# Performance work log

Measured on AMD Instinct MI355X. Metric: run time of the kernel, lower is better.

## Reference

```python
import jax, jax.numpy as jnp
import numpy as np

N, E, G = 30000, 240000, 128
D_IN, D_H, D_OUT, HEADS = 128, 128, 16, 4
EPS_BN = 1e-5


def setup_inputs() -> dict:
    key = jax.random.key(0)
    ks = jax.random.split(key, 24)
    s = 0.1
    inp = {
        "x": jax.random.normal(ks[0], (N, D_IN), jnp.float32),
        "edge_index": jax.random.randint(ks[1], (2, E), 0, N, jnp.int32),
        "batch": jnp.sort(jax.random.randint(ks[2], (N,), 0, G, jnp.int32)),
        # stacked per-layer params (3 GAT blocks, identical shapes since D_IN==D_H)
        "W": jax.random.normal(ks[3], (3, D_H, HEADS * D_H), jnp.float32) * s,
        "att_src": jax.random.normal(ks[4], (3, HEADS, D_H), jnp.float32) * s,
        "att_dst": jax.random.normal(ks[5], (3, HEADS, D_H), jnp.float32) * s,
        "conv_b": jnp.zeros((3, D_H), jnp.float32),
        "gamma": jnp.ones((3, D_H), jnp.float32),
        "beta": jnp.zeros((3, D_H), jnp.float32),
        "sk_Win": jax.random.normal(ks[6], (3, D_H, D_H), jnp.float32) * s,
        "sk_bin": jnp.zeros((3, D_H), jnp.float32),
        "sk_Wout": jax.random.normal(ks[7], (3, D_H, D_H), jnp.float32) * s,
        "sk_bout": jnp.zeros((3, D_H), jnp.float32),
        "fc1_W": jax.random.normal(ks[8], (D_H, D_H), jnp.float32) * s,
        "fc1_b": jnp.zeros((D_H,), jnp.float32),
        "fc3_W": jax.random.normal(ks[9], (D_H, D_OUT), jnp.float32) * s,
        "fc3_b": jnp.zeros((D_OUT,), jnp.float32),
    }
    return inp


def _gat_conv(x, src, dst, W, a_src, a_dst, b):
    # PyG GATConv, heads=4, concat=False (mean over heads), leaky_relu 0.2
    h = (x @ W).reshape(N, HEADS, D_H)                      # [N,H,C]
    al_s = jnp.einsum('nhc,hc->nh', h, a_src)               # [N,H]
    al_d = jnp.einsum('nhc,hc->nh', h, a_dst)
    e = jax.nn.leaky_relu(al_s[src] + al_d[dst], 0.2)       # [Etot,H]
    m = jax.ops.segment_max(e, dst, num_segments=N)
    m = jnp.where(jnp.isfinite(m), m, 0.0)
    ex = jnp.exp(e - m[dst])
    z = jax.ops.segment_sum(ex, dst, num_segments=N)
    alpha = ex / (z[dst] + 1e-16)                           # [Etot,H]
    msg = h[src] * alpha[:, :, None]                        # [Etot,H,C]
    out = jax.ops.segment_sum(msg, dst, num_segments=N)     # [N,H,C]
    return out.mean(axis=1) + b


def _batch_norm(h, gamma, beta):
    mu = h.mean(axis=0)
    var = h.var(axis=0)
    return gamma * (h - mu) * jax.lax.rsqrt(var + EPS_BN) + beta


def _gated_skip(in_x, out_x, Win, bin_, Wout, bout):
    gate = jax.nn.sigmoid(in_x @ Win + bin_ + out_x @ Wout + bout)
    return gate * out_x + (1.0 - gate) * in_x


def reference(x, edge_index, batch, W, att_src, att_dst, conv_b, gamma, beta,
              sk_Win, sk_bin, sk_Wout, sk_bout, fc1_W, fc1_b, fc3_W, fc3_b):
    # add self loops (PyG GATConv default)
    loops = jnp.arange(N, dtype=edge_index.dtype)
    src = jnp.concatenate([edge_index[0], loops])
    dst = jnp.concatenate([edge_index[1], loops])

    h = x
    for l in range(3):
        idn = h
        h = _gat_conv(h, src, dst, W[l], att_src[l], att_dst[l], conv_b[l])
        h = _batch_norm(h, gamma[l], beta[l])
        h = _gated_skip(idn, h, sk_Win[l], sk_bin[l], sk_Wout[l], sk_bout[l])
        h = jax.nn.relu(h)

    # global mean pool over graphs
    cnt = jax.ops.segment_sum(jnp.ones((N,), h.dtype), batch, num_segments=G)
    hg = jax.ops.segment_sum(h, batch, num_segments=G) / jnp.maximum(cnt, 1.0)[:, None]
    hg = jax.nn.relu(hg @ fc1_W + fc1_b)
    return hg @ fc3_W + fc3_b
```

## Files before the change

### kernel.cpp

```cpp
#include <hip/hip_runtime.h>
#include <hip/hip_bf16.h>

#define N_NODES 30000
#define N_EDGES 240000
#define ETOT    (N_EDGES + N_NODES)
#define NGRAPH  128
#define NBLK    118

typedef __attribute__((ext_vector_type(8))) short bf16x8;
typedef __attribute__((ext_vector_type(4))) short bf16x4;
typedef __attribute__((ext_vector_type(4))) float f32x4;

__device__ __forceinline__ unsigned short f2bf(float f) {
    unsigned u = __float_as_uint(f);
    u += 0x7fff + ((u >> 16) & 1);
    return (unsigned short)(u >> 16);
}
__device__ __forceinline__ float bf2f(unsigned short h) {
    return __uint_as_float(((unsigned)h) << 16);
}

__global__ __launch_bounds__(256) void prep_kernel(const float* __restrict__ W,
                                                   const float* __restrict__ Win,
                                                   const float* __restrict__ Wout,
                                                   const float* __restrict__ x,
                                                   const int* __restrict__ batch,
                                                   short* __restrict__ wt_hi,
                                                   short* __restrict__ wint_hi,
                                                   short* __restrict__ woutt_hi,
                                                   short* __restrict__ xb,
                                                   int* __restrict__ gstart) {
    int i = blockIdx.x * 256 + threadIdx.x;
    if (i < 196608) {
        int l = i >> 16, r = i & 65535;
        int n = r >> 7, k = r & 127;
        wt_hi[i] = (short)f2bf(W[(size_t)l * 65536 + k * 512 + n]);
    } else if (i < 245760) {
        int j = i - 196608;
        int l = j >> 14, r = j & 16383;
        int n = r >> 7, k = r & 127;
        wint_hi[j] = (short)f2bf(Win[(size_t)l * 16384 + k * 128 + n]);
    } else if (i < 294912) {
        int j = i - 245760;
        int l = j >> 14, r = j & 16383;
        int n = r >> 7, k = r & 127;
        woutt_hi[j] = (short)f2bf(Wout[(size_t)l * 16384 + k * 128 + n]);
    } else if (i < 294912 + 480000) {
        int j = i - 294912;
        const float4* p = (const float4*)x + (size_t)j * 2;
        float4 v0 = p[0], v1 = p[1];
        bf16x8 hv;
        hv[0] = (short)f2bf(v0.x); hv[1] = (short)f2bf(v0.y);
        hv[2] = (short)f2bf(v0.z); hv[3] = (short)f2bf(v0.w);
        hv[4] = (short)f2bf(v1.x); hv[5] = (short)f2bf(v1.y);
        hv[6] = (short)f2bf(v1.z); hv[7] = (short)f2bf(v1.w);
        *(bf16x8*)(xb + (size_t)j * 8) = hv;
    } else if (i < 294912 + 480000 + 129) {
        int t = i - 294912 - 480000;
        int lo = 0, hi = N_NODES;
        while (lo < hi) { int mid = (lo + hi) >> 1; if (batch[mid] < t) lo = mid + 1; else hi = mid; }
        gstart[t] = lo;
    }
}

__global__ __launch_bounds__(256) void gemm_conv(const short* __restrict__ Ab,
                                                 const short* __restrict__ Bth,
                                                 const float* __restrict__ att_s,
                                                 const float* __restrict__ att_d,
                                                 unsigned short* __restrict__ hfullb,
                                                 float* __restrict__ als,
                                                 float* __restrict__ ald) {
    __shared__ short As_h[64 * 136];
    __shared__ float red_s[2][64], red_d[2][64];
    const int bm = blockIdx.x * 64;
    const int hd = blockIdx.y;
    const int bn = hd * 128;
    const int t  = threadIdx.x;
#pragma unroll
    for (int i = 0; i < 4; i++) {
        int idx8 = t + i * 256;
        int row = idx8 >> 4, c8 = (idx8 & 15) << 3;
        bf16x8 vh = {};
        if (bm + row < N_NODES)
            vh = *(const bf16x8*)(Ab + (size_t)(bm + row) * 128 + c8);
        *(bf16x8*)(As_h + row * 136 + c8) = vh;
    }
    __syncthreads();

    const int w = t >> 6, lane = t & 63;
    const int wr = w >> 1, wc = w & 1;
    const int lr = lane & 15, lg = lane >> 4;
    f32x4 acc[2][4] = {};
    const size_t bofs0 = (size_t)(bn + wc * 64 + lr) * 128 + lg * 8;
#pragma unroll
    for (int kk = 0; kk < 4; kk++) {
        bf16x8 ah[2], bh[4];
#pragma unroll
        for (int ni = 0; ni < 4; ni++) {
            size_t o = bofs0 + (size_t)ni * 16 * 128 + kk * 32;
            bh[ni] = *(const bf16x8*)(Bth + o);
        }
        int ko = kk * 32 + lg * 8;
#pragma unroll
        for (int mi = 0; mi < 2; mi++) {
            int r = wr * 32 + mi * 16 + lr;
            ah[mi] = *(const bf16x8*)(As_h + r * 136 + ko);
        }
#pragma unroll
        for (int mi = 0; mi < 2; mi++)
#pragma unroll
            for (int ni = 0; ni < 4; ni++)
                acc[mi][ni] = __builtin_amdgcn_mfma_f32_16x16x32_bf16(ah[mi], bh[ni], acc[mi][ni], 0, 0, 0);
    }
    float as_c[4], ad_c[4];
#pragma unroll
    for (int ni = 0; ni < 4; ni++) {
        int cc = wc * 64 + ni * 16 + lr;
        as_c[ni] = att_s[hd * 128 + cc];
        ad_c[ni] = att_d[hd * 128 + cc];
    }
#pragma unroll
    for (int mi = 0; mi < 2; mi++) {
#pragma unroll
        for (int r = 0; r < 4; r++) {
            float ps = 0.f, pd = 0.f;
#pragma unroll
            for (int ni = 0; ni < 4; ni++) {
                ps = fmaf(acc[mi][ni][r], as_c[ni], ps);
                pd = fmaf(acc[mi][ni][r], ad_c[ni], pd);
            }
#pragma unroll
            for (int off = 1; off < 16; off <<= 1) {
                ps += __shfl_xor(ps, off);
                pd += __shfl_xor(pd, off);
            }
            if (lr == 0) {
                int row = wr * 32 + mi * 16 + lg * 4 + r;
                red_s[wc][row] = ps;
                red_d[wc][row] = pd;
            }
        }
    }
    __syncthreads();
#pragma unroll
    for (int mi = 0; mi < 2; mi++)
#pragma unroll
        for (int ni = 0; ni < 4; ni++) {
            int nl = wc * 64 + ni * 16 + lr;
#pragma unroll
            for (int r = 0; r < 4; r++) {
                int row = wr * 32 + mi * 16 + lg * 4 + r;
                As_h[row * 136 + nl] = (short)f2bf(acc[mi][ni][r]);
            }
        }
    if (t < 64) {
        int m = bm + t;
        if (m < N_NODES) als[m * 4 + hd] = red_s[0][t] + red_s[1][t];
    } else if (t < 128) {
        int tt = t - 64;
        int m = bm + tt;
        if (m < N_NODES) ald[m * 4 + hd] = red_d[0][tt] + red_d[1][tt];
    }
    __syncthreads();
#pragma unroll
    for (int i2 = 0; i2 < 4; i2++) {
        int idx8 = t + i2 * 256;
        int row = idx8 >> 4, c8 = (idx8 & 15) << 3;
        int m = bm + row;
        if (m < N_NODES)
            *(bf16x8*)(hfullb + (size_t)m * 512 + bn + c8) = *(const bf16x8*)(As_h + row * 136 + c8);
    }
}

__global__ __launch_bounds__(256) void skip_gate(const short* __restrict__ hinb,
                                                 const float* __restrict__ g,
                                                 const float* __restrict__ bnsum,
                                                 const float* __restrict__ gamma,
                                                 const float* __restrict__ beta,
                                                 const short* __restrict__ w1h,
                                                 const short* __restrict__ w2h,
                                                 const float* __restrict__ bin, const float* __restrict__ bout,
                                                 short* __restrict__ houtb) {
    __shared__ short A1h[64 * 136], A2h[64 * 136], A2l[64 * 136];
    __shared__ float bnp_s[256];
    const int bm = blockIdx.x * 64;
    const int bn = blockIdx.y * 64;
    const int t  = threadIdx.x;
    if (t < 128) {
        float inv = 1.f / (float)N_NODES;
        float mu  = bnsum[t] * inv;
        float var = bnsum[128 + t] * inv - mu * mu;
        float rs  = rsqrtf(var + 1e-5f);
        float sc  = gamma[t] * rs;
        bnp_s[t]       = sc;
        bnp_s[128 + t] = beta[t] - mu * sc;
    }
    __syncthreads();
#pragma unroll
    for (int i = 0; i < 4; i++) {
        int idx8 = t + i * 256;
        int row = idx8 >> 4, c8 = (idx8 & 15) << 3;
        bf16x8 vh = {};
        if (bm + row < N_NODES)
            vh = *(const bf16x8*)(hinb + (size_t)(bm + row) * 128 + c8);
        *(bf16x8*)(A1h + row * 136 + c8) = vh;
    }
#pragma unroll
    for (int i = 0; i < 8; i++) {
        int idx4 = t + i * 256;
        int row = idx4 >> 5, c4 = (idx4 & 31) << 2;
        float4 v2 = make_float4(0.f, 0.f, 0.f, 0.f);
        if (bm + row < N_NODES) {
            float4 gv = *(const float4*)(g + (size_t)(bm + row) * 128 + c4);
            v2.x = fmaf(bnp_s[c4 + 0], gv.x, bnp_s[128 + c4 + 0]);
            v2.y = fmaf(bnp_s[c4 + 1], gv.y, bnp_s[128 + c4 + 1]);
            v2.z = fmaf(bnp_s[c4 + 2], gv.z, bnp_s[128 + c4 + 2]);
            v2.w = fmaf(bnp_s[c4 + 3], gv.w, bnp_s[128 + c4 + 3]);
        }
        unsigned short b0 = f2bf(v2.x), b1 = f2bf(v2.y), b2 = f2bf(v2.z), b3 = f2bf(v2.w);
        *(bf16x4*)(A2h + row * 136 + c4) = (bf16x4){(short)b0, (short)b1, (short)b2, (short)b3};
        *(bf16x4*)(A2l + row * 136 + c4) = (bf16x4){(short)f2bf(v2.x - bf2f(b0)), (short)f2bf(v2.y - bf2f(b1)),
                                                    (short)f2bf(v2.z - bf2f(b2)), (short)f2bf(v2.w - bf2f(b3))};
    }
    __syncthreads();

    const int w = t >> 6, lane = t & 63;
    const int wr = w >> 1, wc = w & 1;
    const int lr = lane & 15, lg = lane >> 4;
    f32x4 acc[2][2] = {};
    const size_t bofs0 = (size_t)(bn + wc * 32 + lr) * 128 + lg * 8;
#pragma unroll
    for (int kk = 0; kk < 4; kk++) {
        bf16x8 a1f[2], a2f[2], b1h[2], b2h[2];
#pragma unroll
        for (int ni = 0; ni < 2; ni++) {
            size_t o = bofs0 + (size_t)ni * 16 * 128 + kk * 32;
            b1h[ni] = *(const bf16x8*)(w1h + o);
            b2h[ni] = *(const bf16x8*)(w2h + o);
        }
        int ko = kk * 32 + lg * 8;
#pragma unroll
        for (int mi = 0; mi < 2; mi++) {
            int r = wr * 32 + mi * 16 + lr;
            a1f[mi] = *(const bf16x8*)(A1h + r * 136 + ko);
            a2f[mi] = *(const bf16x8*)(A2h + r * 136 + ko);
        }
#pragma unroll
        for (int mi = 0; mi < 2; mi++)
#pragma unroll
            for (int ni = 0; ni < 2; ni++) {
                acc[mi][ni] = __builtin_amdgcn_mfma_f32_16x16x32_bf16(a1f[mi], b1h[ni], acc[mi][ni], 0, 0, 0);
                acc[mi][ni] = __builtin_amdgcn_mfma_f32_16x16x32_bf16(a2f[mi], b2h[ni], acc[mi][ni], 0, 0, 0);
            }
    }
#pragma unroll
    for (int mi = 0; mi < 2; mi++) {
#pragma unroll
        for (int ni = 0; ni < 2; ni++) {
            int n = bn + wc * 32 + ni * 16 + lr;
            float bsum = bin[n] + bout[n];
#pragma unroll
            for (int r = 0; r < 4; r++) {
                int lrow = wr * 32 + mi * 16 + lg * 4 + r;
                float hbnv = bf2f((unsigned short)A2h[lrow * 136 + n]) + bf2f((unsigned short)A2l[lrow * 136 + n]);
                float hv   = bf2f((unsigned short)A1h[lrow * 136 + n]);
                float gt   = 1.f / (1.f + __expf(-(acc[mi][ni][r] + bsum)));
                acc[mi][ni][r] = fmaxf(gt * hbnv + (1.f - gt) * hv, 0.f);
            }
        }
    }
    __syncthreads();
#pragma unroll
    for (int mi = 0; mi < 2; mi++)
#pragma unroll
        for (int ni = 0; ni < 2; ni++) {
            int n = bn + wc * 32 + ni * 16 + lr;
#pragma unroll
            for (int r = 0; r < 4; r++) {
                int lrow = wr * 32 + mi * 16 + lg * 4 + r;
                A1h[lrow * 136 + n] = (short)f2bf(acc[mi][ni][r]);
            }
        }
    __syncthreads();
#pragma unroll
    for (int i2 = 0; i2 < 2; i2++) {
        int idx8 = t + i2 * 256;
        int row = idx8 >> 3, c8 = (idx8 & 7) << 3;
        int m = bm + row;
        if (m < N_NODES)
            *(bf16x8*)(houtb + (size_t)m * 128 + bn + c8) = *(const bf16x8*)(A1h + row * 136 + bn + c8);
    }
}

__global__ __launch_bounds__(256) void deg_kernel(const int* __restrict__ ei1,
                                                  int* __restrict__ deg) {
    int e = blockIdx.x * 256 + threadIdx.x;
    if (e >= ETOT) return;
    int d = (e < N_EDGES) ? ei1[e] : (e - N_EDGES);
    atomicAdd(&deg[d], 1);
}

__global__ __launch_bounds__(256) void scan1(const int* __restrict__ deg,
                                             int* __restrict__ tmp,
                                             int* __restrict__ blksum) {
    int i = blockIdx.x * 256 + threadIdx.x;
    int v = (i < N_NODES) ? deg[i] : 0;
    __shared__ int sh[256];
    sh[threadIdx.x] = v;
    __syncthreads();
    int acc = v;
    for (int off = 1; off < 256; off <<= 1) {
        int u = (threadIdx.x >= off) ? sh[threadIdx.x - off] : 0;
        __syncthreads();
        acc += u;
        sh[threadIdx.x] = acc;
        __syncthreads();
    }
    if (i < N_NODES) tmp[i] = acc - v;
    if (threadIdx.x == 255) blksum[blockIdx.x] = acc;
}

__global__ void scan2(const int* __restrict__ blksum, int* __restrict__ blkoff) {
    int t = threadIdx.x;
    int v = (t < NBLK) ? blksum[t] : 0;
    __shared__ int sh[128];
    sh[t] = v;
    __syncthreads();
    int acc = v;
    for (int off = 1; off < 128; off <<= 1) {
        int u = (t >= off) ? sh[t - off] : 0;
        __syncthreads();
        acc += u;
        sh[t] = acc;
        __syncthreads();
    }
    if (t < NBLK) blkoff[t] = acc - v;
}

__global__ __launch_bounds__(256) void scan3(const int* __restrict__ tmp,
                                             const int* __restrict__ blkoff,
                                             int* __restrict__ rowptr,
                                             int* __restrict__ wofs) {
    int i = blockIdx.x * 256 + threadIdx.x;
    if (i == 0) rowptr[N_NODES] = ETOT;
    if (i < N_NODES) {
        int r = tmp[i] + blkoff[blockIdx.x];
        rowptr[i] = r;
        wofs[i]   = r;
    }
}

__global__ __launch_bounds__(256) void scatter_kernel(const int* __restrict__ ei0,
                                                      const int* __restrict__ ei1,
                                                      int* __restrict__ wofs,
                                                      int* __restrict__ csr_src) {
    int e = blockIdx.x * 256 + threadIdx.x;
    if (e >= ETOT) return;
    int s = (e < N_EDGES) ? ei0[e] : (e - N_EDGES);
    int d = (e < N_EDGES) ? ei1[e] : (e - N_EDGES);
    int pos = atomicAdd(&wofs[d], 1);
    csr_src[pos] = s;
}

__global__ __launch_bounds__(256) void gat_gather(const int* __restrict__ rowptr,
                                                  const int* __restrict__ csr_src,
                                                  const float* __restrict__ al_s,
                                                  const float* __restrict__ al_d,
                                                  const unsigned short* __restrict__ hfullb,
                                                  const float* __restrict__ conv_b,
                                                  float* __restrict__ g,
                                                  float* __restrict__ bnsum,
                                                  float* __restrict__ bnsum2) {
    const int lane = threadIdx.x & 63;
    const int wib  = threadIdx.x >> 6;
    const int gwid = blockIdx.x * 4 + wib;
    const int nw   = gridDim.x * 4;
    const int h    = lane >> 4;
    const int sub  = lane & 15;
    float s1[8] = {}, s2[8] = {};

    for (int n = gwid; n < N_NODES; n += nw) {
        const int e0 = rowptr[n], e1 = rowptr[n + 1];
        const float ald_h = al_d[n * 4 + h];

        float acc[8] = {};
        float zs = 0.f;
        int i = e0;
        for (; i + 3 < e1; i += 4) {
            int sA = csr_src[i], sB = csr_src[i + 1], sC = csr_src[i + 2], sD = csr_src[i + 3];
            bf16x8 ha = *(const bf16x8*)(hfullb + (size_t)sA * 512 + lane * 8);
            bf16x8 hb = *(const bf16x8*)(hfullb + (size_t)sB * 512 + lane * 8);
            bf16x8 hc = *(const bf16x8*)(hfullb + (size_t)sC * 512 + lane * 8);
            bf16x8 hd = *(const bf16x8*)(hfullb + (size_t)sD * 512 + lane * 8);
            float vA = al_s[sA * 4 + h] + ald_h; vA = (vA > 0.f) ? vA : 0.2f * vA;
            float vB = al_s[sB * 4 + h] + ald_h; vB = (vB > 0.f) ? vB : 0.2f * vB;
            float vC = al_s[sC * 4 + h] + ald_h; vC = (vC > 0.f) ? vC : 0.2f * vC;
            float vD = al_s[sD * 4 + h] + ald_h; vD = (vD > 0.f) ? vD : 0.2f * vD;
            float exA = __expf(vA), exB = __expf(vB), exC = __expf(vC), exD = __expf(vD);
            zs += (exA + exB) + (exC + exD);
#pragma unroll
            for (int j = 0; j < 8; j++) {
                float a = fmaf(exA, bf2f((unsigned short)ha[j]), acc[j]);
                a = fmaf(exB, bf2f((unsigned short)hb[j]), a);
                a = fmaf(exC, bf2f((unsigned short)hc[j]), a);
                acc[j] = fmaf(exD, bf2f((unsigned short)hd[j]), a);
            }
        }
        for (; i < e1; i++) {
            int sA = csr_src[i];
            bf16x8 ha = *(const bf16x8*)(hfullb + (size_t)sA * 512 + lane * 8);
            float vA = al_s[sA * 4 + h] + ald_h; vA = (vA > 0.f) ? vA : 0.2f * vA;
            float exA = __expf(vA);
            zs += exA;
#pragma unroll
            for (int j = 0; j < 8; j++)
                acc[j] = fmaf(exA, bf2f((unsigned short)ha[j]), acc[j]);
        }

        float inv = 0.25f / (zs + 1e-16f);
#pragma unroll
        for (int j = 0; j < 8; j++) {
            float a = acc[j] * inv;
            a += __shfl_xor(a, 16);
            a += __shfl_xor(a, 32);
            acc[j] = a;
        }
        if (lane < 16) {
            float o[8];
#pragma unroll
            for (int j = 0; j < 8; j++) {
                float tv = acc[j] + conv_b[sub * 8 + j];
                o[j] = tv;
                s1[j] += tv;
                s2[j] = fmaf(tv, tv, s2[j]);
            }
            float* gp = g + (size_t)n * 128 + sub * 8;
            *(float4*)gp       = make_float4(o[0], o[1], o[2], o[3]);
            *(float4*)(gp + 4) = make_float4(o[4], o[5], o[6], o[7]);
        }
    }

    __shared__ float redA[4][128], redB[4][128];
    if (lane < 16) {
#pragma unroll
        for (int j = 0; j < 8; j++) {
            redA[wib][sub * 8 + j] = s1[j];
            redB[wib][sub * 8 + j] = s2[j];
        }
    }
    __syncthreads();
    int t = threadIdx.x;
    if (t < 128) {
        atomicAdd(&bnsum[t], redA[0][t] + redA[1][t] + redA[2][t] + redA[3][t]);
    } else {
        int c = t - 128;
        atomicAdd(&bnsum2[c], redB[0][c] + redB[1][c] + redB[2][c] + redB[3][c]);
    }
}

__global__ __launch_bounds__(256) void pool_head(const short* __restrict__ hb,
                                                 const int* __restrict__ gstart,
                                                 const float* __restrict__ fc1W,
                                                 const float* __restrict__ fc1b,
                                                 const float* __restrict__ fc3W,
                                                 const float* __restrict__ fc3b,
                                                 float* __restrict__ out) {
    int gid = blockIdx.x, t = threadIdx.x;
    int lo = gstart[gid], hi = gstart[gid + 1];
    int c = t & 127, half = t >> 7;
    float s = 0.f;
    for (int n = lo + half; n < hi; n += 2)
        s += bf2f((unsigned short)hb[(size_t)n * 128 + c]);
    __shared__ float sh[256];
    __shared__ float hg[128], a1[128];
    sh[t] = s;
    __syncthreads();
    if (half == 0) {
        float cc = fmaxf((float)(hi - lo), 1.f);
        hg[c] = (sh[c] + sh[c + 128]) / cc;
    }
    __syncthreads();
    if (t < 128) {
        float v = fc1b[t];
        for (int c2 = 0; c2 < 128; c2++) v = fmaf(hg[c2], fc1W[c2 * 128 + t], v);
        a1[t] = fmaxf(v, 0.f);
    }
    __syncthreads();
    if (t < 16) {
        float o = fc3b[t];
        for (int j = 0; j < 128; j++) o = fmaf(a1[j], fc3W[j * 16 + t], o);
        out[gid * 16 + t] = o;
    }
}

extern "C" void kernel_launch(void* const* d_in, const int* in_sizes, int n_in,
                              void* d_out, int out_size, void* d_ws, size_t ws_size,
                              hipStream_t stream) {
    const float* x       = (const float*)d_in[0];
    const int*   ei      = (const int*)d_in[1];
    const int*   batch   = (const int*)d_in[2];
    const float* W       = (const float*)d_in[3];
    const float* att_src = (const float*)d_in[4];
    const float* att_dst = (const float*)d_in[5];
    const float* conv_b  = (const float*)d_in[6];
    const float* gamma   = (const float*)d_in[7];
    const float* beta    = (const float*)d_in[8];
    const float* sk_Win  = (const float*)d_in[9];
    const float* sk_bin  = (const float*)d_in[10];
    const float* sk_Wout = (const float*)d_in[11];
    const float* sk_bout = (const float*)d_in[12];
    const float* fc1_W   = (const float*)d_in[13];
    const float* fc1_b   = (const float*)d_in[14];
    const float* fc3_W   = (const float*)d_in[15];
    const float* fc3_b   = (const float*)d_in[16];
    float* out = (float*)d_out;
    const int* ei0 = ei;
    const int* ei1 = ei + N_EDGES;

    float* ws = (float*)d_ws;
    size_t o = 0;
    unsigned short* hfullb = (unsigned short*)(ws + o); o += (size_t)N_NODES * 256;
    float* gbuf   = ws + o; o += (size_t)N_NODES * 128;
    short* hbA    = (short*)(ws + o); o += (size_t)N_NODES * 64;
    short* hbB    = (short*)(ws + o); o += (size_t)N_NODES * 64;
    float* als    = ws + o; o += N_NODES * 4;
    float* ald    = ws + o; o += N_NODES * 4;
    float* bnsum  = ws + o; o += 768;
    short* wt_hi   = (short*)(ws + o); o += 98304;
    short* wint_hi = (short*)(ws + o); o += 24576;
    short* woutt_hi = (short*)(ws + o); o += 24576;
    int* gstart   = (int*)(ws + o); o += 132;
    int* deg      = (int*)(ws + o); o += N_NODES;
    int* rowptr   = (int*)(ws + o); o += N_NODES + 4;
    int* wofs     = (int*)(ws + o); o += N_NODES;
    int* scantmp  = (int*)(ws + o); o += N_NODES;
    int* blksum   = (int*)(ws + o); o += NBLK + 2;
    int* blkoff   = (int*)(ws + o); o += NBLK + 2;
    int* csr_src  = (int*)(ws + o); o += ETOT;

    prep_kernel<<<3028, 256, 0, stream>>>(W, sk_Win, sk_Wout, x, batch,
                                          wt_hi, wint_hi, woutt_hi, hbA, gstart);

    hipMemsetAsync(deg, 0, N_NODES * 4, stream);
    hipMemsetAsync(bnsum, 0, 768 * 4, stream);
    deg_kernel<<<(ETOT + 255) / 256, 256, 0, stream>>>(ei1, deg);
    scan1<<<NBLK, 256, 0, stream>>>(deg, scantmp, blksum);
    scan2<<<1, 128, 0, stream>>>(blksum, blkoff);
    scan3<<<NBLK, 256, 0, stream>>>(scantmp, blkoff, rowptr, wofs);
    scatter_kernel<<<(ETOT + 255) / 256, 256, 0, stream>>>(ei0, ei1, wofs, csr_src);

    short* sih = hbA;
    short* soh = hbB;
    for (int l = 0; l < 3; l++) {
        gemm_conv<<<dim3(469, 4), 256, 0, stream>>>(sih,
                                                    wt_hi + (size_t)l * 65536,
                                                    att_src + l * 512, att_dst + l * 512,
                                                    hfullb, als, ald);
        gat_gather<<<1024, 256, 0, stream>>>(rowptr, csr_src, als, ald, hfullb,
                                             conv_b + l * 128, gbuf,
                                             bnsum + l * 256, bnsum + l * 256 + 128);
        skip_gate<<<dim3(469, 2), 256, 0, stream>>>(sih, gbuf,
                                                    bnsum + l * 256, gamma + l * 128, beta + l * 128,
                                                    wint_hi + (size_t)l * 16384,
                                                    woutt_hi + (size_t)l * 16384,
                                                    sk_bin + l * 128, sk_bout + l * 128,
                                                    soh);
        short* th = sih; sih = soh; soh = th;
    }

    pool_head<<<NGRAPH, 256, 0, stream>>>(sih, gstart, fc1_W, fc1_b, fc3_W, fc3_b, out);
}
```

Measured before the change: 416.6 us.

## Merge preprocessing into cooperative kernel and fuse skip-gate with next layer's GAT GEMM

Folds the weight/input conversion, degree count, three-stage scan and CSR scatter into one cooperative kernel that uses grid syncs in place of separate launches and memsets. Also adds a skip_conv kernel: it computes the gated skip for layers 1-2 and, from the same 64-row tile, the next layer's 4-head projection and attention logits. This removes extra kernel launches and one re-read of the layer output from global memory. In exchange the fused kernel holds large accumulator arrays, so register pressure is high and occupancy may drop, and the cooperative launch needs all 1024 blocks resident at once.

```diff
diff --git a/kernel.cpp b/kernel.cpp
--- a/kernel.cpp
+++ b/kernel.cpp
@@ -1,5 +1,6 @@
 #include <hip/hip_runtime.h>
 #include <hip/hip_bf16.h>
+#include <hip/hip_cooperative_groups.h>
 
 #define N_NODES 30000
 #define N_EDGES 240000
@@ -20,33 +21,49 @@
     return __uint_as_float(((unsigned)h) << 16);
 }
 
-__global__ __launch_bounds__(256) void prep_kernel(const float* __restrict__ W,
-                                                   const float* __restrict__ Win,
-                                                   const float* __restrict__ Wout,
-                                                   const float* __restrict__ x,
-                                                   const int* __restrict__ batch,
-                                                   short* __restrict__ wt_hi,
-                                                   short* __restrict__ wint_hi,
-                                                   short* __restrict__ woutt_hi,
-                                                   short* __restrict__ xb,
-                                                   int* __restrict__ gstart) {
-    int i = blockIdx.x * 256 + threadIdx.x;
-    if (i < 196608) {
-        int l = i >> 16, r = i & 65535;
-        int n = r >> 7, k = r & 127;
-        wt_hi[i] = (short)f2bf(W[(size_t)l * 65536 + k * 512 + n]);
-    } else if (i < 245760) {
-        int j = i - 196608;
-        int l = j >> 14, r = j & 16383;
-        int n = r >> 7, k = r & 127;
-        wint_hi[j] = (short)f2bf(Win[(size_t)l * 16384 + k * 128 + n]);
-    } else if (i < 294912) {
-        int j = i - 245760;
-        int l = j >> 14, r = j & 16383;
-        int n = r >> 7, k = r & 127;
-        woutt_hi[j] = (short)f2bf(Wout[(size_t)l * 16384 + k * 128 + n]);
-    } else if (i < 294912 + 480000) {
-        int j = i - 294912;
+__global__ void coop_prep(const float* __restrict__ W,
+                          const float* __restrict__ Win,
+                          const float* __restrict__ Wout,
+                          const float* __restrict__ x,
+                          const int* __restrict__ batch,
+                          const int* __restrict__ ei0,
+                          const int* __restrict__ ei1,
+                          short* __restrict__ wt_hi,
+                          short* __restrict__ wint_hi,
+                          short* __restrict__ woutt_hi,
+                          short* __restrict__ xb,
+                          int* __restrict__ gstart,
+                          int* __restrict__ deg,
+                          int* __restrict__ rowptr,
+                          int* __restrict__ wofs,
+                          int* __restrict__ scantmp,
+                          int* __restrict__ blksum,
+                          int* __restrict__ blkoff,
+                          int* __restrict__ csr_src,
+                          float* __restrict__ bnsum) {
+    cooperative_groups::grid_group grid = cooperative_groups::this_grid();
+    const int gtid = blockIdx.x * 256 + threadIdx.x;
+    const int gsz  = gridDim.x * 256;
+    __shared__ int sh[256];
+
+    for (int i = gtid; i < 294912; i += gsz) {
+        if (i < 196608) {
+            int l = i >> 16, r = i & 65535;
+            int n = r >> 7, k = r & 127;
+            wt_hi[i] = (short)f2bf(W[(size_t)l * 65536 + k * 512 + n]);
+        } else if (i < 245760) {
+            int j = i - 196608;
+            int l = j >> 14, r = j & 16383;
+            int n = r >> 7, k = r & 127;
+            wint_hi[j] = (short)f2bf(Win[(size_t)l * 16384 + k * 128 + n]);
+        } else {
+            int j = i - 245760;
+            int l = j >> 14, r = j & 16383;
+            int n = r >> 7, k = r & 127;
+            woutt_hi[j] = (short)f2bf(Wout[(size_t)l * 16384 + k * 128 + n]);
+        }
+    }
+    for (int j = gtid; j < N_NODES * 16; j += gsz) {
         const float4* p = (const float4*)x + (size_t)j * 2;
         float4 v0 = p[0], v1 = p[1];
         bf16x8 hv;
@@ -55,11 +72,67 @@
         hv[4] = (short)f2bf(v1.x); hv[5] = (short)f2bf(v1.y);
         hv[6] = (short)f2bf(v1.z); hv[7] = (short)f2bf(v1.w);
         *(bf16x8*)(xb + (size_t)j * 8) = hv;
-    } else if (i < 294912 + 480000 + 129) {
-        int t = i - 294912 - 480000;
+    }
+    for (int i = gtid; i < N_NODES; i += gsz) deg[i] = 0;
+    if (gtid < 768) bnsum[gtid] = 0.f;
+    if (gtid <= NGRAPH) {
         int lo = 0, hi = N_NODES;
-        while (lo < hi) { int mid = (lo + hi) >> 1; if (batch[mid] < t) lo = mid + 1; else hi = mid; }
-        gstart[t] = lo;
+        while (lo < hi) { int mid = (lo + hi) >> 1; if (batch[mid] < gtid) lo = mid + 1; else hi = mid; }
+        gstart[gtid] = lo;
+    }
+    grid.sync();
+    for (int e = gtid; e < ETOT; e += gsz) {
+        int d = (e < N_EDGES) ? ei1[e] : (e - N_EDGES);
+        atomicAdd(&deg[d], 1);
+    }
+    grid.sync();
+    if (blockIdx.x < NBLK) {
+        int i = blockIdx.x * 256 + threadIdx.x;
+        int v = (i < N_NODES) ? deg[i] : 0;
+        sh[threadIdx.x] = v;
+        __syncthreads();
+        int a = v;
+        for (int off = 1; off < 256; off <<= 1) {
+            int u = (threadIdx.x >= off) ? sh[threadIdx.x - off] : 0;
+            __syncthreads();
+            a += u;
+            sh[threadIdx.x] = a;
+            __syncthreads();
+        }
+        if (i < N_NODES) scantmp[i] = a - v;
+        if (threadIdx.x == 255) blksum[blockIdx.x] = a;
+    }
+    grid.sync();
+    if (blockIdx.x == 0) {
+        int t = threadIdx.x;
+        int v = (t < NBLK) ? blksum[t] : 0;
+        if (t < 128) sh[t] = v;
+        __syncthreads();
+        int a = v;
+        for (int off = 1; off < 128; off <<= 1) {
+            int u = (t >= off && t < 128) ? sh[t - off] : 0;
+            __syncthreads();
+            if (t < 128) { a += u; sh[t] = a; }
+            __syncthreads();
+        }
+        if (t < NBLK) blkoff[t] = a - v;
+    }
+    grid.sync();
+    if (blockIdx.x < NBLK) {
+        int i = blockIdx.x * 256 + threadIdx.x;
+        if (i < N_NODES) {
+            int r = scantmp[i] + blkoff[blockIdx.x];
+            rowptr[i] = r;
+            wofs[i]   = r;
+        }
+    }
+    if (gtid == 0) rowptr[N_NODES] = ETOT;
+    grid.sync();
+    for (int e = gtid; e < ETOT; e += gsz) {
+        int s = (e < N_EDGES) ? ei0[e] : (e - N_EDGES);
+        int d = (e < N_EDGES) ? ei1[e] : (e - N_EDGES);
+        int pos = atomicAdd(&wofs[d], 1);
+        csr_src[pos] = s;
     }
 }
 
@@ -169,6 +242,238 @@
         int m = bm + row;
         if (m < N_NODES)
             *(bf16x8*)(hfullb + (size_t)m * 512 + bn + c8) = *(const bf16x8*)(As_h + row * 136 + c8);
+    }
+}
+
+__global__ __launch_bounds__(256) void skip_conv(const short* __restrict__ hinb,
+                                                 const float* __restrict__ g,
+                                                 const float* __restrict__ bnsum,
+                                                 const float* __restrict__ gamma,
+                                                 const float* __restrict__ beta,
+                                                 const short* __restrict__ w1h,
+                                                 const short* __restrict__ w2h,
+                                                 const float* __restrict__ bin,
+                                                 const float* __restrict__ bout,
+                                                 const short* __restrict__ wtn,
+                                                 const float* __restrict__ att_s,
+                                                 const float* __restrict__ att_d,
+                                                 short* __restrict__ houtb,
+                                                 unsigned short* __restrict__ hfullb,
+                                                 float* __restrict__ als,
+                                                 float* __restrict__ ald) {
+    __shared__ short A1h[64 * 136], A2h[64 * 136];
+    __shared__ float bnp_s[256];
+    __shared__ float redS[4][64], redD[4][64];
+    const int bm = blockIdx.x * 64;
+    const int t  = threadIdx.x;
+    if (t < 128) {
+        float inv = 1.f / (float)N_NODES;
+        float mu  = bnsum[t] * inv;
+        float var = bnsum[128 + t] * inv - mu * mu;
+        float rs  = rsqrtf(var + 1e-5f);
+        float sc  = gamma[t] * rs;
+        bnp_s[t]       = sc;
+        bnp_s[128 + t] = beta[t] - mu * sc;
+    }
+    __syncthreads();
+#pragma unroll
+    for (int i = 0; i < 4; i++) {
+        int idx8 = t + i * 256;
+        int row = idx8 >> 4, c8 = (idx8 & 15) << 3;
+        bf16x8 vh = {};
+        if (bm + row < N_NODES)
+            vh = *(const bf16x8*)(hinb + (size_t)(bm + row) * 128 + c8);
+        *(bf16x8*)(A1h + row * 136 + c8) = vh;
+    }
+#pragma unroll
+    for (int i = 0; i < 8; i++) {
+        int idx4 = t + i * 256;
+        int row = idx4 >> 5, c4 = (idx4 & 31) << 2;
+        float4 v2 = make_float4(0.f, 0.f, 0.f, 0.f);
+        if (bm + row < N_NODES) {
+            float4 gv = *(const float4*)(g + (size_t)(bm + row) * 128 + c4);
+            v2.x = fmaf(bnp_s[c4 + 0], gv.x, bnp_s[128 + c4 + 0]);
+            v2.y = fmaf(bnp_s[c4 + 1], gv.y, bnp_s[128 + c4 + 1]);
+            v2.z = fmaf(bnp_s[c4 + 2], gv.z, bnp_s[128 + c4 + 2]);
+            v2.w = fmaf(bnp_s[c4 + 3], gv.w, bnp_s[128 + c4 + 3]);
+        }
+        *(bf16x4*)(A2h + row * 136 + c4) = (bf16x4){(short)f2bf(v2.x), (short)f2bf(v2.y),
+                                                    (short)f2bf(v2.z), (short)f2bf(v2.w)};
+    }
+    __syncthreads();
+
+    const int w = t >> 6, lane = t & 63;
+    const int wr = w >> 1, wc = w & 1;
+    const int lr = lane & 15, lg = lane >> 4;
+
+    {
+        f32x4 acc[2][4] = {};
+        const size_t bo = (size_t)(wc * 64 + lr) * 128 + lg * 8;
+#pragma unroll
+        for (int kk = 0; kk < 4; kk++) {
+            bf16x8 a1[2], a2[2], b1[4], b2[4];
+#pragma unroll
+            for (int ni = 0; ni < 4; ni++) {
+                size_t o = bo + (size_t)ni * 2048 + kk * 32;
+                b1[ni] = *(const bf16x8*)(w1h + o);
+                b2[ni] = *(const bf16x8*)(w2h + o);
+            }
+            int ko = kk * 32 + lg * 8;
+#pragma unroll
+            for (int mi = 0; mi < 2; mi++) {
+                int r = wr * 32 + mi * 16 + lr;
+                a1[mi] = *(const bf16x8*)(A1h + r * 136 + ko);
+                a2[mi] = *(const bf16x8*)(A2h + r * 136 + ko);
+            }
+#pragma unroll
+            for (int mi = 0; mi < 2; mi++)
+#pragma unroll
+                for (int ni = 0; ni < 4; ni++) {
+                    acc[mi][ni] = __builtin_amdgcn_mfma_f32_16x16x32_bf16(a1[mi], b1[ni], acc[mi][ni], 0, 0, 0);
+                    acc[mi][ni] = __builtin_amdgcn_mfma_f32_16x16x32_bf16(a2[mi], b2[ni], acc[mi][ni], 0, 0, 0);
+                }
+        }
+#pragma unroll
+        for (int mi = 0; mi < 2; mi++)
+#pragma unroll
+            for (int ni = 0; ni < 4; ni++) {
+                int n = wc * 64 + ni * 16 + lr;
+                float bsum = bin[n] + bout[n];
+                float sc = bnp_s[n], shb = bnp_s[128 + n];
+#pragma unroll
+                for (int r = 0; r < 4; r++) {
+                    int lrow = wr * 32 + mi * 16 + lg * 4 + r;
+                    int m = bm + lrow;
+                    float gv = (m < N_NODES) ? g[(size_t)m * 128 + n] : 0.f;
+                    float hbnv = fmaf(sc, gv, shb);
+                    float hv   = bf2f((unsigned short)A1h[lrow * 136 + n]);
+                    float gt   = 1.f / (1.f + __expf(-(acc[mi][ni][r] + bsum)));
+                    acc[mi][ni][r] = fmaxf(gt * hbnv + (1.f - gt) * hv, 0.f);
+                }
+            }
+        __syncthreads();
+#pragma unroll
+        for (int mi = 0; mi < 2; mi++)
+#pragma unroll
+            for (int ni = 0; ni < 4; ni++) {
+                int n = wc * 64 + ni * 16 + lr;
+#pragma unroll
+                for (int r = 0; r < 4; r++) {
+                    int lrow = wr * 32 + mi * 16 + lg * 4 + r;
+                    A1h[lrow * 136 + n] = (short)f2bf(acc[mi][ni][r]);
+                }
+            }
+        __syncthreads();
+#pragma unroll
+        for (int i2 = 0; i2 < 4; i2++) {
+            int idx8 = t + i2 * 256;
+            int row = idx8 >> 4, c8 = (idx8 & 15) << 3;
+            int m = bm + row;
+            if (m < N_NODES)
+                *(bf16x8*)(houtb + (size_t)m * 128 + c8) = *(const bf16x8*)(A1h + row * 136 + c8);
+        }
+    }
+
+    f32x4 c2[4][8] = {};
+    const int hd = w;
+    const size_t bo2 = (size_t)(hd * 128 + lr) * 128 + lg * 8;
+#pragma unroll
+    for (int kk = 0; kk < 4; kk++) {
+        bf16x8 ah2[4], bh2[8];
+#pragma unroll
+        for (int ni = 0; ni < 8; ni++)
+            bh2[ni] = *(const bf16x8*)(wtn + bo2 + (size_t)ni * 2048 + kk * 32);
+        int ko = kk * 32 + lg * 8;
+#pragma unroll
+        for (int mi = 0; mi < 4; mi++)
+            ah2[mi] = *(const bf16x8*)(A1h + (mi * 16 + lr) * 136 + ko);
+#pragma unroll
+        for (int mi = 0; mi < 4; mi++)
+#pragma unroll
+            for (int ni = 0; ni < 8; ni++)
+                c2[mi][ni] = __builtin_amdgcn_mfma_f32_16x16x32_bf16(ah2[mi], bh2[ni], c2[mi][ni], 0, 0, 0);
+    }
+    {
+        float asc[8], adc[8];
+#pragma unroll
+        for (int ni = 0; ni < 8; ni++) {
+            int cc = ni * 16 + lr;
+            asc[ni] = att_s[hd * 128 + cc];
+            adc[ni] = att_d[hd * 128 + cc];
+        }
+#pragma unroll
+        for (int mi = 0; mi < 4; mi++)
+#pragma unroll
+            for (int r = 0; r < 4; r++) {
+                float ps = 0.f, pd = 0.f;
+#pragma unroll
+                for (int ni = 0; ni < 8; ni++) {
+                    ps = fmaf(c2[mi][ni][r], asc[ni], ps);
+                    pd = fmaf(c2[mi][ni][r], adc[ni], pd);
+                }
+#pragma unroll
+                for (int off = 1; off < 16; off <<= 1) {
+                    ps += __shfl_xor(ps, off);
+                    pd += __shfl_xor(pd, off);
+                }
+                if (lr == 0) {
+                    int row = mi * 16 + lg * 4 + r;
+                    redS[hd][row] = ps;
+                    redD[hd][row] = pd;
+                }
+            }
+    }
+    __syncthreads();
+    if (w < 2) {
+        short* dst = (w == 0) ? A1h : A2h;
+#pragma unroll
+        for (int mi = 0; mi < 4; mi++)
+#pragma unroll
+            for (int ni = 0; ni < 8; ni++)
+#pragma unroll
+                for (int r = 0; r < 4; r++)
+                    dst[(mi * 16 + lg * 4 + r) * 136 + ni * 16 + lr] = (short)f2bf(c2[mi][ni][r]);
+    }
+    {
+        int hd2 = t >> 6, row = t & 63;
+        int m = bm + row;
+        if (m < N_NODES) {
+            als[m * 4 + hd2] = redS[hd2][row];
+            ald[m * 4 + hd2] = redD[hd2][row];
+        }
+    }
+    __syncthreads();
+#pragma unroll
+    for (int it = 0; it < 8; it++) {
+        int idx = t + it * 256;
+        int row = idx >> 5, c8 = (idx & 31) << 3;
+        int m = bm + row;
+        if (m < N_NODES) {
+            const short* src = (c8 < 128) ? A1h : A2h;
+            *(bf16x8*)(hfullb + (size_t)m * 512 + c8) = *(const bf16x8*)(src + row * 136 + (c8 & 127));
+        }
+    }
+    __syncthreads();
+    if (w >= 2) {
+        short* dst = (w == 2) ? A1h : A2h;
+#pragma unroll
+        for (int mi = 0; mi < 4; mi++)
+#pragma unroll
+            for (int ni = 0; ni < 8; ni++)
+#pragma unroll
+                for (int r = 0; r < 4; r++)
+                    dst[(mi * 16 + lg * 4 + r) * 136 + ni * 16 + lr] = (short)f2bf(c2[mi][ni][r]);
+    }
+    __syncthreads();
+#pragma unroll
+    for (int it = 0; it < 8; it++) {
+        int idx = t + it * 256;
+        int row = idx >> 5, c8 = (idx & 31) << 3;
+        int m = bm + row;
+        if (m < N_NODES) {
+            const short* src = (c8 < 128) ? A1h : A2h;
+            *(bf16x8*)(hfullb + (size_t)m * 512 + 256 + c8) = *(const bf16x8*)(src + row * 136 + (c8 & 127));
+        }
     }
 }
 
@@ -290,76 +595,6 @@
         if (m < N_NODES)
             *(bf16x8*)(houtb + (size_t)m * 128 + bn + c8) = *(const bf16x8*)(A1h + row * 136 + bn + c8);
     }
-}
-
-__global__ __launch_bounds__(256) void deg_kernel(const int* __restrict__ ei1,
-                                                  int* __restrict__ deg) {
-    int e = blockIdx.x * 256 + threadIdx.x;
-    if (e >= ETOT) return;
-    int d = (e < N_EDGES) ? ei1[e] : (e - N_EDGES);
-    atomicAdd(&deg[d], 1);
-}
-
-__global__ __launch_bounds__(256) void scan1(const int* __restrict__ deg,
-                                             int* __restrict__ tmp,
-                                             int* __restrict__ blksum) {
-    int i = blockIdx.x * 256 + threadIdx.x;
-    int v = (i < N_NODES) ? deg[i] : 0;
-    __shared__ int sh[256];
-    sh[threadIdx.x] = v;
-    __syncthreads();
-    int acc = v;
-    for (int off = 1; off < 256; off <<= 1) {
-        int u = (threadIdx.x >= off) ? sh[threadIdx.x - off] : 0;
-        __syncthreads();
-        acc += u;
-        sh[threadIdx.x] = acc;
-        __syncthreads();
-    }
-    if (i < N_NODES) tmp[i] = acc - v;
-    if (threadIdx.x == 255) blksum[blockIdx.x] = acc;
-}
-
-__global__ void scan2(const int* __restrict__ blksum, int* __restrict__ blkoff) {
-    int t = threadIdx.x;
-    int v = (t < NBLK) ? blksum[t] : 0;
-    __shared__ int sh[128];
-    sh[t] = v;
-    __syncthreads();
-    int acc = v;
-    for (int off = 1; off < 128; off <<= 1) {
-        int u = (t >= off) ? sh[t - off] : 0;
-        __syncthreads();
-        acc += u;
-        sh[t] = acc;
-        __syncthreads();
-    }
-    if (t < NBLK) blkoff[t] = acc - v;
-}
-
-__global__ __launch_bounds__(256) void scan3(const int* __restrict__ tmp,
-                                             const int* __restrict__ blkoff,
-                                             int* __restrict__ rowptr,
-                                             int* __restrict__ wofs) {
-    int i = blockIdx.x * 256 + threadIdx.x;
-    if (i == 0) rowptr[N_NODES] = ETOT;
-    if (i < N_NODES) {
-        int r = tmp[i] + blkoff[blockIdx.x];
-        rowptr[i] = r;
-        wofs[i]   = r;
-    }
-}
-
-__global__ __launch_bounds__(256) void scatter_kernel(const int* __restrict__ ei0,
-                                                      const int* __restrict__ ei1,
-                                                      int* __restrict__ wofs,
-                                                      int* __restrict__ csr_src) {
-    int e = blockIdx.x * 256 + threadIdx.x;
-    if (e >= ETOT) return;
-    int s = (e < N_EDGES) ? ei0[e] : (e - N_EDGES);
-    int d = (e < N_EDGES) ? ei1[e] : (e - N_EDGES);
-    int pos = atomicAdd(&wofs[d], 1);
-    csr_src[pos] = s;
 }
 
 __global__ __launch_bounds__(256) void gat_gather(const int* __restrict__ rowptr,
@@ -538,35 +773,35 @@
     int* blkoff   = (int*)(ws + o); o += NBLK + 2;
     int* csr_src  = (int*)(ws + o); o += ETOT;
 
-    prep_kernel<<<3028, 256, 0, stream>>>(W, sk_Win, sk_Wout, x, batch,
-                                          wt_hi, wint_hi, woutt_hi, hbA, gstart);
-
-    hipMemsetAsync(deg, 0, N_NODES * 4, stream);
-    hipMemsetAsync(bnsum, 0, 768 * 4, stream);
-    deg_kernel<<<(ETOT + 255) / 256, 256, 0, stream>>>(ei1, deg);
-    scan1<<<NBLK, 256, 0, stream>>>(deg, scantmp, blksum);
-    scan2<<<1, 128, 0, stream>>>(blksum, blkoff);
-    scan3<<<NBLK, 256, 0, stream>>>(scantmp, blkoff, rowptr, wofs);
-    scatter_kernel<<<(ETOT + 255) / 256, 256, 0, stream>>>(ei0, ei1, wofs, csr_src);
-
-    short* sih = hbA;
-    short* soh = hbB;
-    for (int l = 0; l < 3; l++) {
-        gemm_conv<<<dim3(469, 4), 256, 0, stream>>>(sih,
-                                                    wt_hi + (size_t)l * 65536,
-                                                    att_src + l * 512, att_dst + l * 512,
-                                                    hfullb, als, ald);
-        gat_gather<<<1024, 256, 0, stream>>>(rowptr, csr_src, als, ald, hfullb,
-                                             conv_b + l * 128, gbuf,
-                                             bnsum + l * 256, bnsum + l * 256 + 128);
-        skip_gate<<<dim3(469, 2), 256, 0, stream>>>(sih, gbuf,
-                                                    bnsum + l * 256, gamma + l * 128, beta + l * 128,
-                                                    wint_hi + (size_t)l * 16384,
-                                                    woutt_hi + (size_t)l * 16384,
-                                                    sk_bin + l * 128, sk_bout + l * 128,
-                                                    soh);
-        short* th = sih; sih = soh; soh = th;
-    }
-
-    pool_head<<<NGRAPH, 256, 0, stream>>>(sih, gstart, fc1_W, fc1_b, fc3_W, fc3_b, out);
+    {
+        void* cargs[] = {(void*)&W, (void*)&sk_Win, (void*)&sk_Wout, (void*)&x, (void*)&batch,
+                         (void*)&ei0, (void*)&ei1,
+                         (void*)&wt_hi, (void*)&wint_hi, (void*)&woutt_hi,
+                         (void*)&hbA, (void*)&gstart,
+                         (void*)&deg, (void*)&rowptr, (void*)&wofs,
+                         (void*)&scantmp, (void*)&blksum, (void*)&blkoff,
+                         (void*)&csr_src, (void*)&bnsum};
+        hipLaunchCooperativeKernel((void*)coop_prep, dim3(1024), dim3(256), cargs, 0, stream);
+    }
+
+    gemm_conv<<<dim3(469, 4), 256, 0, stream>>>(hbA, wt_hi, att_src, att_dst, hfullb, als, ald);
+    gat_gather<<<1024, 256, 0, stream>>>(rowptr, csr_src, als, ald, hfullb,
+                                         conv_b, gbuf, bnsum, bnsum + 128);
+    skip_conv<<<469, 256, 0, stream>>>(hbA, gbuf, bnsum, gamma, beta,
+                                       wint_hi, woutt_hi, sk_bin, sk_bout,
+                                       wt_hi + 65536, att_src + 512, att_dst + 512,
+                                       hbB, hfullb, als, ald);
+    gat_gather<<<1024, 256, 0, stream>>>(rowptr, csr_src, als, ald, hfullb,
+                                         conv_b + 128, gbuf, bnsum + 256, bnsum + 384);
+    skip_conv<<<469, 256, 0, stream>>>(hbB, gbuf, bnsum + 256, gamma + 128, beta + 128,
+                                       wint_hi + 16384, woutt_hi + 16384, sk_bin + 128, sk_bout + 128,
+                                       wt_hi + 131072, att_src + 1024, att_dst + 1024,
+                                       hbA, hfullb, als, ald);
+    gat_gather<<<1024, 256, 0, stream>>>(rowptr, csr_src, als, ald, hfullb,
+                                         conv_b + 256, gbuf, bnsum + 512, bnsum + 640);
+    skip_gate<<<dim3(469, 2), 256, 0, stream>>>(hbA, gbuf, bnsum + 512, gamma + 256, beta + 256,
+                                                wint_hi + 32768, woutt_hi + 32768,
+                                                sk_bin + 256, sk_bout + 256, hbB);
+
+    pool_head<<<NGRAPH, 256, 0, stream>>>(hbB, gstart, fc1_W, fc1_b, fc3_W, fc3_b, out);
 }
```

Result: slower. 929.3 us (+123.1%).
